# Performance work log

Hardware: AMD Instinct MI355X
Metric: run time of the kernel (lower is better)

## Reference

```python
import jax, jax.numpy as jnp
import numpy as np

B, F, V, D, K = 16384, 39, 30000, 16, 20
EPS = 1e-5


def bn_eval(x, g, b):
    # inference-mode BatchNorm1d with running_mean=0, running_var=1
    return g * x / jnp.sqrt(1.0 + EPS) + b


def setup_inputs() -> dict:
    key = jax.random.key(0)
    ks = jax.random.split(key, 12)
    x = jax.random.randint(ks[0], (B, F), 0, V)
    emb_table = jax.random.normal(ks[1], (F * V, D), dtype=jnp.float32) * 0.05
    w_c = jax.random.normal(ks[2], (F, F * D), dtype=jnp.float32) * 0.05
    w0 = jax.random.normal(ks[3], (1024, F * D), dtype=jnp.float32) * 0.04
    w1 = jax.random.normal(ks[4], (512, 1024), dtype=jnp.float32) * 0.03
    w_out = jax.random.normal(ks[5], (1, 512), dtype=jnp.float32) * 0.04
    return {
        'x': x, 'emb_table': emb_table,
        'w_c': w_c, 'b_c': jnp.zeros((F,)), 'g_c': jnp.ones((F,)), 'be_c': jnp.zeros((F,)),
        'w0': w0, 'b0': jnp.zeros((1024,)), 'g0': jnp.ones((1024,)), 'be0': jnp.zeros((1024,)),
        'w1': w1, 'b1': jnp.zeros((512,)), 'g1': jnp.ones((512,)), 'be1': jnp.zeros((512,)),
        'w_out': w_out, 'b_out': jnp.zeros((1,)),
    }


def reference(x, emb_table, w_c, b_c, g_c, be_c, w0, b0, g0, be0,
              w1, b1, g1, be1, w_out, b_out):
    offsets = jnp.arange(F, dtype=x.dtype) * V          # per-field offsets
    idx = x + offsets[None, :]                          # [B, F]
    emb = emb_table[idx]                                # [B, F, D] gather

    # controller_mlp: flatten (batch, D, F) layout like torch transpose(1,2)
    flat = jnp.transpose(emb, (0, 2, 1)).reshape(B, F * D)
    h = jax.nn.relu(bn_eval(flat @ w_c.T + b_c, g_c, be_c))
    scores = jax.nn.softmax(h, axis=1)                  # [B, F]

    # kmax_pooling: top-k field indices, sorted ascending, gather weights
    _, kidx = jax.lax.top_k(scores, K)
    kidx = jnp.sort(kidx, axis=1)                       # [B, K]
    w = jnp.take_along_axis(scores, kidx, axis=1)       # [B, K]

    # forward_select: gather selected field embeddings, weight them
    sel = jnp.take_along_axis(emb, kidx[:, :, None], axis=1)  # [B, K, D]
    weighted = sel * w[:, :, None]

    # scatter back into full field slots (unselected fields are zero)
    full = jnp.zeros((B, F, D), weighted.dtype)
    bidx = jnp.arange(B)[:, None]
    full = full.at[bidx, kidx].set(weighted)            # [B, F, D]

    z = jnp.transpose(full, (0, 2, 1)).reshape(B, F * D)
    z = jax.nn.relu(bn_eval(z @ w0.T + b0, g0, be0))
    z = jax.nn.relu(bn_eval(z @ w1.T + b1, g1, be1))
    out = jax.nn.sigmoid(z @ w_out.T + b_out)           # [B, 1]
    return out.squeeze(-1)
```

## Files before the change

kernel.cpp:

```cpp
#include <hip/hip_runtime.h>
#include <math.h>

#define B_SZ 16384
#define F_N 39
#define V_N 30000
#define D_N 16
#define K_SEL 20
#define FD 624
#define KP0 640
#define NCP 48
#define N0 1024
#define N1 512
#define CBR 16
#define ALD 648

typedef unsigned short u16;
typedef __attribute__((ext_vector_type(8))) short bf16x8;
typedef __attribute__((ext_vector_type(8))) unsigned short u16x8;
typedef __attribute__((ext_vector_type(4))) float f32x4;
typedef __attribute__((ext_vector_type(4))) unsigned short u16x4;

__device__ __forceinline__ u16 f2bf(float v) {
    union { float f; unsigned u; } x; x.f = v;
    unsigned r = x.u + 0x7fff + ((x.u >> 16) & 1);
    return (u16)(r >> 16);
}
__device__ __forceinline__ float bf2f(u16 v) {
    union { unsigned u; float f; } x; x.u = ((unsigned)v) << 16;
    return x.f;
}

#define GLD16(gp, lp) __builtin_amdgcn_global_load_lds( \
    (const __attribute__((address_space(1))) unsigned int*)(gp), \
    (__attribute__((address_space(3))) unsigned int*)(lp), 16, 0, 0)

#define PREP_W0 (N0 * KP0)
#define PREP_W1 (N1 * N0)
#define PREP_WC (NCP * KP0)
#define PREP_TOT (PREP_W0 + PREP_W1 + PREP_WC + 3 * NCP)

__global__ __launch_bounds__(256) void prep_all_kernel(
    const float* __restrict__ w0, const float* __restrict__ w1,
    const float* __restrict__ w_c, const float* __restrict__ b_c,
    const float* __restrict__ g_c, const float* __restrict__ be_c,
    u16* __restrict__ w0b, u16* __restrict__ w1b, u16* __restrict__ wcb,
    float* __restrict__ bcp, float* __restrict__ gcp, float* __restrict__ becp)
{
    int i = blockIdx.x * blockDim.x + threadIdx.x;
    if (i < PREP_W0) {
        int n = i / KP0, kk = i - n * KP0;
        float v = 0.f;
        if (kk < FD) v = w0[n * FD + (kk & 15) * F_N + (kk >> 4)];
        w0b[i] = f2bf(v);
        return;
    }
    i -= PREP_W0;
    if (i < PREP_W1) { w1b[i] = f2bf(w1[i]); return; }
    i -= PREP_W1;
    if (i < PREP_WC) {
        int n = i / KP0, kk = i - n * KP0;
        float v = 0.f;
        if (n < F_N && kk < FD) v = w_c[n * FD + (kk & 15) * F_N + (kk >> 4)];
        wcb[i] = f2bf(v);
        return;
    }
    i -= PREP_WC;
    if (i < 3 * NCP) {
        int which = i / NCP, n = i - which * NCP;
        float v = 0.f;
        if (n < F_N) v = (which == 0) ? b_c[n] : (which == 1) ? g_c[n] : be_c[n];
        ((which == 0) ? bcp : (which == 1) ? gcp : becp)[n] = v;
    }
}

__global__ __launch_bounds__(256) void fused_controller_kernel(
    const int* __restrict__ x, const float* __restrict__ emb_table,
    const u16* __restrict__ wcb, const float* __restrict__ bcp,
    const float* __restrict__ gcp, const float* __restrict__ becp,
    u16* __restrict__ zb)
{
    __shared__ __align__(16) u16 Al[CBR * ALD];
    __shared__ float vv[CBR][49];
    __shared__ f32x4 part[4][64][3];
    __shared__ float selw[CBR][F_N];

    const int t    = threadIdx.x;
    const int wave = t >> 6;
    const int lane = t & 63;
    const int b0   = blockIdx.x * CBR;

    for (int p = t; p < CBR * F_N; p += 256) {
        const int row = p / F_N;
        const int f   = p - row * F_N;
        const int xi  = x[b0 * F_N + p];
        const float4* src = (const float4*)(emb_table + (size_t)(xi + f * V_N) * D_N);
        float4 v0 = src[0], v1 = src[1], v2 = src[2], v3 = src[3];
        u16x8 o0 = { f2bf(v0.x), f2bf(v0.y), f2bf(v0.z), f2bf(v0.w),
                     f2bf(v1.x), f2bf(v1.y), f2bf(v1.z), f2bf(v1.w) };
        u16x8 o1 = { f2bf(v2.x), f2bf(v2.y), f2bf(v2.z), f2bf(v2.w),
                     f2bf(v3.x), f2bf(v3.y), f2bf(v3.z), f2bf(v3.w) };
        *(u16x8*)&Al[row * ALD + f * D_N]     = o0;
        *(u16x8*)&Al[row * ALD + f * D_N + 8] = o1;
    }
    __syncthreads();

    const int m = lane & 15;
    const int q = lane >> 4;
    f32x4 acc0 = {}, acc1 = {}, acc2 = {};
    {
        const u16* ap  = &Al[m * ALD + wave * 160 + q * 8];
        const u16* bp0 = wcb + (size_t)(0  + m) * KP0 + wave * 160 + q * 8;
        const u16* bp1 = wcb + (size_t)(16 + m) * KP0 + wave * 160 + q * 8;
        const u16* bp2 = wcb + (size_t)(32 + m) * KP0 + wave * 160 + q * 8;
        #pragma unroll
        for (int k = 0; k < 5; ++k) {
            bf16x8 af = *(const bf16x8*)ap;
            bf16x8 b0 = *(const bf16x8*)bp0;
            bf16x8 b1 = *(const bf16x8*)bp1;
            bf16x8 b2 = *(const bf16x8*)bp2;
            acc0 = __builtin_amdgcn_mfma_f32_16x16x32_bf16(af, b0, acc0, 0, 0, 0);
            acc1 = __builtin_amdgcn_mfma_f32_16x16x32_bf16(af, b1, acc1, 0, 0, 0);
            acc2 = __builtin_amdgcn_mfma_f32_16x16x32_bf16(af, b2, acc2, 0, 0, 0);
            ap += 32; bp0 += 32; bp1 += 32; bp2 += 32;
        }
    }
    part[wave][lane][0] = acc0;
    part[wave][lane][1] = acc1;
    part[wave][lane][2] = acc2;
    __syncthreads();

    {
        f32x4 r0 = part[0][lane][0] + part[1][lane][0] + part[2][lane][0] + part[3][lane][0];
        f32x4 r1 = part[0][lane][1] + part[1][lane][1] + part[2][lane][1] + part[3][lane][1];
        f32x4 r2 = part[0][lane][2] + part[1][lane][2] + part[2][lane][2] + part[3][lane][2];

        const float rs = rsqrtf(1.0f + 1e-5f);
        if (q == wave) {
            #pragma unroll
            for (int j = 0; j < 3; ++j) {
                const f32x4 a = (j == 0) ? r0 : (j == 1) ? r1 : r2;
                const int n = j * 16 + m;
                const float gn = gcp[n] * rs;
                const float bn = becp[n];
                const float bi = bcp[n];
                #pragma unroll
                for (int r = 0; r < 4; ++r)
                    vv[wave * 4 + r][n] = fmaxf(fmaf(gn, a[r] + bi, bn), 0.f);
            }
        }
    }
    __syncthreads();

    {
        const int row = wave * 4 + (lane >> 4);
        const int fl  = lane & 15;
        float e[3] = {0.f, 0.f, 0.f};
        float mloc = -1e30f;
        #pragma unroll
        for (int it = 0; it < 3; ++it) {
            const int f = fl + 16 * it;
            if (f < F_N) { e[it] = vv[row][f]; mloc = fmaxf(mloc, e[it]); }
        }
        mloc = fmaxf(mloc, __shfl_xor(mloc, 1, 64));
        mloc = fmaxf(mloc, __shfl_xor(mloc, 2, 64));
        mloc = fmaxf(mloc, __shfl_xor(mloc, 4, 64));
        mloc = fmaxf(mloc, __shfl_xor(mloc, 8, 64));
        float sloc = 0.f;
        #pragma unroll
        for (int it = 0; it < 3; ++it) {
            const int f = fl + 16 * it;
            if (f < F_N) { e[it] = expf(e[it] - mloc); sloc += e[it]; }
        }
        sloc += __shfl_xor(sloc, 1, 64);
        sloc += __shfl_xor(sloc, 2, 64);
        sloc += __shfl_xor(sloc, 4, 64);
        sloc += __shfl_xor(sloc, 8, 64);
        const float inv = 1.f / sloc;
        #pragma unroll
        for (int it = 0; it < 3; ++it) {
            const int f = fl + 16 * it;
            if (f < F_N) vv[row][f] = e[it];
        }

        int rank[3] = {};
        for (int gg = 0; gg < F_N; ++gg) {
            const float o = vv[row][gg];
            #pragma unroll
            for (int it = 0; it < 3; ++it) {
                const int f = fl + 16 * it;
                if (f < F_N)
                    rank[it] += (o > e[it] || (o == e[it] && gg < f)) ? 1 : 0;
            }
        }
        #pragma unroll
        for (int it = 0; it < 3; ++it) {
            const int f = fl + 16 * it;
            if (f < F_N)
                selw[row][f] = (rank[it] < K_SEL) ? e[it] * inv : 0.f;
        }
    }
    __syncthreads();

    for (int gp = t; gp < CBR * 40; gp += 256) {
        const int row  = gp & 15;
        const int slot = gp >> 4;
        u16* dst = zb + (size_t)(b0 + row) * KP0 + slot * D_N;
        u16x8 o0 = {0,0,0,0,0,0,0,0}, o1 = {0,0,0,0,0,0,0,0};
        if (slot < F_N) {
            const float w = selw[row][slot];
            u16x8 a0 = *(u16x8*)&Al[row * ALD + slot * D_N];
            u16x8 a1 = *(u16x8*)&Al[row * ALD + slot * D_N + 8];
            #pragma unroll
            for (int k = 0; k < 8; ++k) {
                o0[k] = f2bf(bf2f(a0[k]) * w);
                o1[k] = f2bf(bf2f(a1[k]) * w);
            }
        }
        *(u16x8*)dst = o0;
        *(u16x8*)(dst + 8) = o1;
    }
}

template<int MODE>
__global__ __launch_bounds__(256) void gemm_mfma_bn_relu(
    const u16* __restrict__ A, const u16* __restrict__ W,
    const float* __restrict__ bias, const float* __restrict__ g,
    const float* __restrict__ be, u16* __restrict__ Cout,
    int M, int N, int Kp,
    const float* __restrict__ w_out, float* __restrict__ outp)
{
    __shared__ __align__(16) u16 As[2][128 * 32];
    __shared__ __align__(16) u16 Bs[2][128 * 32];

    const int t    = threadIdx.x;
    const int wave = t >> 6;
    const int lane = t & 63;
    const int wm   = wave >> 1, wn = wave & 1;
    const int m0   = blockIdx.x * 128;
    const int n0   = blockIdx.y * 128;

    const int lr    = lane >> 2;
    const int swz_u = (lane & 3) ^ ((lane >> 3) & 3);
    const u16* gA0 = A + (size_t)(m0 + wave * 32 + lr) * Kp + swz_u * 8;
    const u16* gB0 = W + (size_t)(n0 + wave * 32 + lr) * Kp + swz_u * 8;
    const size_t kstep16 = 16 * (size_t)Kp;
    const int oA0 = (wave * 32) * 32;
    const int oA1 = (wave * 32 + 16) * 32;

    const int q    = lane >> 4;
    const int lr16 = lane & 15;

    int aoff[4], boff[4];
    #pragma unroll
    for (int i = 0; i < 4; ++i) {
        int ra = wm * 64 + i * 16 + lr16;
        aoff[i] = ra * 32 + ((q ^ ((ra >> 1) & 3)) * 8);
        int rb = wn * 64 + i * 16 + lr16;
        boff[i] = rb * 32 + ((q ^ ((rb >> 1) & 3)) * 8);
    }

    GLD16(gA0,           &As[0][oA0]);
    GLD16(gA0 + kstep16, &As[0][oA1]);
    GLD16(gB0,           &Bs[0][oA0]);
    GLD16(gB0 + kstep16, &Bs[0][oA1]);
    gA0 += 32; gB0 += 32;

    f32x4 acc[4][4] = {};
    int buf = 0;

    for (int k0 = 0; k0 < Kp; k0 += 32) {
        __syncthreads();
        if (k0 + 32 < Kp) {
            GLD16(gA0,           &As[buf ^ 1][oA0]);
            GLD16(gA0 + kstep16, &As[buf ^ 1][oA1]);
            GLD16(gB0,           &Bs[buf ^ 1][oA0]);
            GLD16(gB0 + kstep16, &Bs[buf ^ 1][oA1]);
            gA0 += 32; gB0 += 32;
        }

        bf16x8 af[4], bfr[4];
        #pragma unroll
        for (int i = 0; i < 4; ++i) af[i]  = *(const bf16x8*)&As[buf][aoff[i]];
        #pragma unroll
        for (int j = 0; j < 4; ++j) bfr[j] = *(const bf16x8*)&Bs[buf][boff[j]];

        #pragma unroll
        for (int i = 0; i < 4; ++i)
            #pragma unroll
            for (int j = 0; j < 4; ++j)
                acc[i][j] = __builtin_amdgcn_mfma_f32_16x16x32_bf16(
                    af[i], bfr[j], acc[i][j], 0, 0, 0);
        buf ^= 1;
    }

    const float rs = rsqrtf(1.0f + 1e-5f);
    if (MODE == 0) {
        #pragma unroll
        for (int j = 0; j < 4; ++j) {
            const int n = n0 + wn * 64 + j * 16 + lr16;
            const float bn_g = g[n] * rs;
            const float bn_b = be[n];
            const float bi   = bias[n];
            #pragma unroll
            for (int i = 0; i < 4; ++i) {
                const int mbase = m0 + wm * 64 + i * 16 + q * 4;
                #pragma unroll
                for (int r = 0; r < 4; ++r) {
                    float v = acc[i][j][r] + bi;
                    v = fmaxf(fmaf(bn_g, v, bn_b), 0.f);
                    Cout[(size_t)(mbase + r) * N + n] = f2bf(v);
                }
            }
        }
    } else {
        float s[4][4] = {};
        #pragma unroll
        for (int j = 0; j < 4; ++j) {
            const int n = n0 + wn * 64 + j * 16 + lr16;
            const float bn_g = g[n] * rs;
            const float bn_b = be[n];
            const float bi   = bias[n];
            const float wo   = w_out[n];
            #pragma unroll
            for (int i = 0; i < 4; ++i)
                #pragma unroll
                for (int r = 0; r < 4; ++r) {
                    float v = acc[i][j][r] + bi;
                    v = fmaxf(fmaf(bn_g, v, bn_b), 0.f);
                    s[i][r] = fmaf(v, wo, s[i][r]);
                }
        }
        #pragma unroll
        for (int i = 0; i < 4; ++i)
            #pragma unroll
            for (int r = 0; r < 4; ++r) {
                float v = s[i][r];
                v += __shfl_xor(v, 1, 64);
                v += __shfl_xor(v, 2, 64);
                v += __shfl_xor(v, 4, 64);
                v += __shfl_xor(v, 8, 64);
                s[i][r] = v;
            }
        if (lr16 == 0) {
            #pragma unroll
            for (int i = 0; i < 4; ++i) {
                const int mbase = m0 + wm * 64 + i * 16 + q * 4;
                #pragma unroll
                for (int r = 0; r < 4; ++r)
                    atomicAdd(&outp[mbase + r], s[i][r]);
            }
        }
    }
}

__global__ __launch_bounds__(256) void sigmoid_kernel(
    const float* __restrict__ outp, const float* __restrict__ b_out,
    float* __restrict__ out)
{
    const int b = blockIdx.x * 256 + threadIdx.x;
    out[b] = 1.f / (1.f + expf(-(outp[b] + b_out[0])));
}

extern "C" void kernel_launch(void* const* d_in, const int* in_sizes, int n_in,
                              void* d_out, int out_size, void* d_ws, size_t ws_size,
                              hipStream_t stream)
{
    const int*   x     = (const int*)  d_in[0];
    const float* emb   = (const float*)d_in[1];
    const float* w_c   = (const float*)d_in[2];
    const float* b_c   = (const float*)d_in[3];
    const float* g_c   = (const float*)d_in[4];
    const float* be_c  = (const float*)d_in[5];
    const float* w0    = (const float*)d_in[6];
    const float* b0    = (const float*)d_in[7];
    const float* g0    = (const float*)d_in[8];
    const float* be0   = (const float*)d_in[9];
    const float* w1    = (const float*)d_in[10];
    const float* b1    = (const float*)d_in[11];
    const float* g1    = (const float*)d_in[12];
    const float* be1   = (const float*)d_in[13];
    const float* w_out = (const float*)d_in[14];
    const float* b_out = (const float*)d_in[15];
    float* out = (float*)d_out;

    u16*   zb    = (u16*)d_ws;
    u16*   w0b   = zb    + (size_t)B_SZ * KP0;
    u16*   h0b   = w0b   + (size_t)N0 * KP0;
    u16*   w1b   = h0b   + (size_t)B_SZ * N0;
    u16*   wcb   = w1b   + (size_t)N1 * N0;
    float* outp  = (float*)(wcb + (size_t)NCP * KP0);
    float* bcp   = outp + B_SZ;
    float* gcp   = bcp + NCP;
    float* becp  = gcp + NCP;

    prep_all_kernel<<<(PREP_TOT + 255) / 256, 256, 0, stream>>>(
        w0, w1, w_c, b_c, g_c, be_c, w0b, w1b, wcb, bcp, gcp, becp);

    fused_controller_kernel<<<B_SZ / CBR, 256, 0, stream>>>(
        x, emb, wcb, bcp, gcp, becp, zb);

    gemm_mfma_bn_relu<0><<<dim3(B_SZ / 128, N0 / 128), 256, 0, stream>>>(
        zb, w0b, b0, g0, be0, h0b, B_SZ, N0, KP0, nullptr, nullptr);

    hipMemsetAsync(outp, 0, B_SZ * sizeof(float), stream);

    gemm_mfma_bn_relu<1><<<dim3(B_SZ / 128, N1 / 128), 256, 0, stream>>>(
        h0b, w1b, b1, g1, be1, nullptr, B_SZ, N1, N0, w_out, outp);

    sigmoid_kernel<<<B_SZ / 256, 256, 0, stream>>>(outp, b_out, out);
}
```

Before: 223.3 us.

## Load GEMM weight fragments directly from global and fold memset into prep

The GEMM kernel no longer stages the weight (B) tile through LDS. Each wave reads its B fragments straight from global memory into registers every k-step, while A keeps double-buffered LDS staging. K is now a template parameter so the k-loop can be fully unrolled. The hipMemsetAsync of the output accumulator is folded into the prep kernel, removing one launch. The aim is to halve LDS traffic and footprint for better occupancy, at the cost of redundant, less-coalesced global loads of W that rely on L2/L1 hits and may expose latency.

Result: slower. 257.2 us (+15.2%).

```diff
diff --git a/kernel.cpp b/kernel.cpp
--- a/kernel.cpp
+++ b/kernel.cpp
@@ -37,14 +37,15 @@
 #define PREP_W0 (N0 * KP0)
 #define PREP_W1 (N1 * N0)
 #define PREP_WC (NCP * KP0)
-#define PREP_TOT (PREP_W0 + PREP_W1 + PREP_WC + 3 * NCP)
+#define PREP_TOT (PREP_W0 + PREP_W1 + PREP_WC + 3 * NCP + B_SZ)
 
 __global__ __launch_bounds__(256) void prep_all_kernel(
     const float* __restrict__ w0, const float* __restrict__ w1,
     const float* __restrict__ w_c, const float* __restrict__ b_c,
     const float* __restrict__ g_c, const float* __restrict__ be_c,
     u16* __restrict__ w0b, u16* __restrict__ w1b, u16* __restrict__ wcb,
-    float* __restrict__ bcp, float* __restrict__ gcp, float* __restrict__ becp)
+    float* __restrict__ bcp, float* __restrict__ gcp, float* __restrict__ becp,
+    float* __restrict__ outp)
 {
     int i = blockIdx.x * blockDim.x + threadIdx.x;
     if (i < PREP_W0) {
@@ -70,7 +71,10 @@
         float v = 0.f;
         if (n < F_N) v = (which == 0) ? b_c[n] : (which == 1) ? g_c[n] : be_c[n];
         ((which == 0) ? bcp : (which == 1) ? gcp : becp)[n] = v;
-    }
+        return;
+    }
+    i -= 3 * NCP;
+    if (i < B_SZ) outp[i] = 0.f;
 }
 
 __global__ __launch_bounds__(256) void fused_controller_kernel(
@@ -221,16 +225,15 @@
     }
 }
 
-template<int MODE>
+template<int MODE, int KP>
 __global__ __launch_bounds__(256) void gemm_mfma_bn_relu(
     const u16* __restrict__ A, const u16* __restrict__ W,
     const float* __restrict__ bias, const float* __restrict__ g,
     const float* __restrict__ be, u16* __restrict__ Cout,
-    int M, int N, int Kp,
+    int M, int N,
     const float* __restrict__ w_out, float* __restrict__ outp)
 {
     __shared__ __align__(16) u16 As[2][128 * 32];
-    __shared__ __align__(16) u16 Bs[2][128 * 32];
 
     const int t    = threadIdx.x;
     const int wave = t >> 6;
@@ -241,48 +244,43 @@
 
     const int lr    = lane >> 2;
     const int swz_u = (lane & 3) ^ ((lane >> 3) & 3);
-    const u16* gA0 = A + (size_t)(m0 + wave * 32 + lr) * Kp + swz_u * 8;
-    const u16* gB0 = W + (size_t)(n0 + wave * 32 + lr) * Kp + swz_u * 8;
-    const size_t kstep16 = 16 * (size_t)Kp;
+    const u16* gA = A + (size_t)(m0 + wave * 32 + lr) * KP + swz_u * 8;
     const int oA0 = (wave * 32) * 32;
     const int oA1 = (wave * 32 + 16) * 32;
 
     const int q    = lane >> 4;
     const int lr16 = lane & 15;
 
-    int aoff[4], boff[4];
+    int aoff[4];
+    const u16* bp[4];
     #pragma unroll
     for (int i = 0; i < 4; ++i) {
         int ra = wm * 64 + i * 16 + lr16;
         aoff[i] = ra * 32 + ((q ^ ((ra >> 1) & 3)) * 8);
-        int rb = wn * 64 + i * 16 + lr16;
-        boff[i] = rb * 32 + ((q ^ ((rb >> 1) & 3)) * 8);
-    }
-
-    GLD16(gA0,           &As[0][oA0]);
-    GLD16(gA0 + kstep16, &As[0][oA1]);
-    GLD16(gB0,           &Bs[0][oA0]);
-    GLD16(gB0 + kstep16, &Bs[0][oA1]);
-    gA0 += 32; gB0 += 32;
+        bp[i] = W + (size_t)(n0 + wn * 64 + i * 16 + lr16) * KP + q * 8;
+    }
+
+    GLD16(gA,           &As[0][oA0]);
+    GLD16(gA + 16 * KP, &As[0][oA1]);
 
     f32x4 acc[4][4] = {};
-    int buf = 0;
-
-    for (int k0 = 0; k0 < Kp; k0 += 32) {
+
+    #pragma unroll
+    for (int it = 0; it < KP / 32; ++it) {
+        const int k0  = it * 32;
+        const int buf = it & 1;
         __syncthreads();
-        if (k0 + 32 < Kp) {
-            GLD16(gA0,           &As[buf ^ 1][oA0]);
-            GLD16(gA0 + kstep16, &As[buf ^ 1][oA1]);
-            GLD16(gB0,           &Bs[buf ^ 1][oA0]);
-            GLD16(gB0 + kstep16, &Bs[buf ^ 1][oA1]);
-            gA0 += 32; gB0 += 32;
-        }
-
-        bf16x8 af[4], bfr[4];
-        #pragma unroll
-        for (int i = 0; i < 4; ++i) af[i]  = *(const bf16x8*)&As[buf][aoff[i]];
-        #pragma unroll
-        for (int j = 0; j < 4; ++j) bfr[j] = *(const bf16x8*)&Bs[buf][boff[j]];
+        if (it + 1 < KP / 32) {
+            GLD16(gA + (k0 + 32),           &As[buf ^ 1][oA0]);
+            GLD16(gA + (k0 + 32) + 16 * KP, &As[buf ^ 1][oA1]);
+        }
+
+        bf16x8 bfr[4];
+        #pragma unroll
+        for (int j = 0; j < 4; ++j) bfr[j] = *(const bf16x8*)(bp[j] + k0);
+        bf16x8 af[4];
+        #pragma unroll
+        for (int i = 0; i < 4; ++i) af[i] = *(const bf16x8*)&As[buf][aoff[i]];
 
         #pragma unroll
         for (int i = 0; i < 4; ++i)
@@ -290,7 +288,6 @@
             for (int j = 0; j < 4; ++j)
                 acc[i][j] = __builtin_amdgcn_mfma_f32_16x16x32_bf16(
                     af[i], bfr[j], acc[i][j], 0, 0, 0);
-        buf ^= 1;
     }
 
     const float rs = rsqrtf(1.0f + 1e-5f);
@@ -394,18 +391,16 @@
     float* becp  = gcp + NCP;
 
     prep_all_kernel<<<(PREP_TOT + 255) / 256, 256, 0, stream>>>(
-        w0, w1, w_c, b_c, g_c, be_c, w0b, w1b, wcb, bcp, gcp, becp);
+        w0, w1, w_c, b_c, g_c, be_c, w0b, w1b, wcb, bcp, gcp, becp, outp);
 
     fused_controller_kernel<<<B_SZ / CBR, 256, 0, stream>>>(
         x, emb, wcb, bcp, gcp, becp, zb);
 
-    gemm_mfma_bn_relu<0><<<dim3(B_SZ / 128, N0 / 128), 256, 0, stream>>>(
-        zb, w0b, b0, g0, be0, h0b, B_SZ, N0, KP0, nullptr, nullptr);
-
-    hipMemsetAsync(outp, 0, B_SZ * sizeof(float), stream);
-
-    gemm_mfma_bn_relu<1><<<dim3(B_SZ / 128, N1 / 128), 256, 0, stream>>>(
-        h0b, w1b, b1, g1, be1, nullptr, B_SZ, N1, N0, w_out, outp);
+    gemm_mfma_bn_relu<0, KP0><<<dim3(B_SZ / 128, N0 / 128), 256, 0, stream>>>(
+        zb, w0b, b0, g0, be0, h0b, B_SZ, N0, nullptr, nullptr);
+
+    gemm_mfma_bn_relu<1, N0><<<dim3(B_SZ / 128, N1 / 128), 256, 0, stream>>>(
+        h0b, w1b, b1, g1, be1, nullptr, B_SZ, N1, w_out, outp);
 
     sigmoid_kernel<<<B_SZ / 256, 256, 0, stream>>>(outp, b_out, out);
 }
```
